# Optimization experiments

Hardware: AMD Instinct MI355X
Metric: run time of the kernel (lower is better)

Reference implementation:

```python
import jax, jax.numpy as jnp
import numpy as np

H = 8  # head_number
NEG = -1e30


def setup_inputs() -> dict:
    key = jax.random.key(0)
    ks = jax.random.split(key, 12)
    B, D, L = 32, 1024, 1024
    s = 1.0 / np.sqrt(D)
    x = jax.random.normal(ks[0], (B, D, L), dtype=jnp.float32)
    mask = jax.random.randint(ks[1], (B, L), 0, 2, dtype=jnp.int32)
    wq = jax.random.normal(ks[2], (D, D), dtype=jnp.float32) * s
    bq = jnp.zeros((D,), dtype=jnp.float32)
    wk = jax.random.normal(ks[3], (D, D), dtype=jnp.float32) * s
    bk = jnp.zeros((D,), dtype=jnp.float32)
    wv = jax.random.normal(ks[4], (D, D), dtype=jnp.float32) * s
    bv = jnp.zeros((D,), dtype=jnp.float32)
    wo = jax.random.normal(ks[5], (D, D), dtype=jnp.float32) * s
    bo = jnp.zeros((D,), dtype=jnp.float32)
    return {"x": x, "mask": mask, "wq": wq, "bq": bq, "wk": wk, "bk": bk,
            "wv": wv, "bv": bv, "wo": wo, "bo": bo}


def reference(x, mask, wq, bq, wk, bk, wv, bv, wo, bo):
    # x: [B, D, L]; mask: [B, L] with 1 = masked (pad). Dropout in eval mode (identity).
    B, D, L = x.shape
    dh = D // H
    scale = 1.0 / np.sqrt(dh)
    xt = jnp.swapaxes(x, 1, 2)  # [B, L, D]
    q = (xt @ wq.T + bq).reshape(B, L, H, dh)
    k = (xt @ wk.T + bk).reshape(B, L, H, dh)
    v = (xt @ wv.T + bv).reshape(B, L, H, dh)
    scores = jnp.einsum('bqhd,bkhd->bhqk', q, k) * scale  # [B, H, L, L]
    m = mask.astype(scores.dtype)[:, None, None, :]  # broadcast over heads, query pos
    scores = scores * (1.0 - m) + m * NEG
    attn = jax.nn.softmax(scores, axis=-1)
    out = jnp.einsum('bhqk,bkhd->bqhd', attn, v).reshape(B, L, D)
    out = out @ wo.T + bo
    return jnp.swapaxes(out, 1, 2)  # [B, D, L]
```

## Files before the change

kernel.cpp:

```cpp
#include <hip/hip_runtime.h>
#include <hip/hip_bf16.h>

typedef __bf16 bf16_t;
typedef bf16_t bf16x8 __attribute__((ext_vector_type(8)));
typedef float f32x4 __attribute__((ext_vector_type(4)));

#define MFMA16(a, b, c) __builtin_amdgcn_mfma_f32_16x16x32_bf16(a, b, c, 0, 0, 0)
#define NEGV -1e30f

__device__ __forceinline__ unsigned short f2bf(float f) {
  union { float f; unsigned int u; } v; v.f = f;
  unsigned int r = v.u + 0x7FFFu + ((v.u >> 16) & 1u);
  return (unsigned short)(r >> 16);
}

__device__ __forceinline__ void gload16(const unsigned short* g, unsigned short* l) {
  __builtin_amdgcn_global_load_lds(
      (const __attribute__((address_space(1))) void*)g,
      (__attribute__((address_space(3))) void*)l, 16, 0, 0);
}

__global__ __launch_bounds__(256) void x_transpose(
    const float* __restrict__ x, unsigned short* __restrict__ xT)
{
  const int b = blockIdx.z;
  const int l0 = blockIdx.x * 64, d0 = blockIdx.y * 64;
  __shared__ __align__(16) unsigned short T[64][68];
  const int tid = threadIdx.x;
  const int dl = tid >> 4, lc = (tid & 15) * 4;
#pragma unroll
  for (int rep = 0; rep < 4; ++rep) {
    int d = dl + rep * 16;
    float4 v = *reinterpret_cast<const float4*>(
        x + ((size_t)b * 1024 + d0 + d) * 1024 + l0 + lc);
    ushort4 u;
    u.x = f2bf(v.x); u.y = f2bf(v.y); u.z = f2bf(v.z); u.w = f2bf(v.w);
    *reinterpret_cast<ushort4*>(&T[d][lc]) = u;
  }
  __syncthreads();
  const int dbase = (tid & 15) * 4, lbase = (tid >> 4) * 4;
  ushort4 r0 = *reinterpret_cast<const ushort4*>(&T[dbase + 0][lbase]);
  ushort4 r1 = *reinterpret_cast<const ushort4*>(&T[dbase + 1][lbase]);
  ushort4 r2 = *reinterpret_cast<const ushort4*>(&T[dbase + 2][lbase]);
  ushort4 r3 = *reinterpret_cast<const ushort4*>(&T[dbase + 3][lbase]);
  ushort4 w0 = {r0.x, r1.x, r2.x, r3.x};
  ushort4 w1 = {r0.y, r1.y, r2.y, r3.y};
  ushort4 w2 = {r0.z, r1.z, r2.z, r3.z};
  ushort4 w3 = {r0.w, r1.w, r2.w, r3.w};
  unsigned short* op = xT + ((size_t)b * 1024 + l0 + lbase) * 1024 + d0 + dbase;
  *reinterpret_cast<ushort4*>(op) = w0;
  *reinterpret_cast<ushort4*>(op + 1024) = w1;
  *reinterpret_cast<ushort4*>(op + 2048) = w2;
  *reinterpret_cast<ushort4*>(op + 3072) = w3;
}

__global__ __launch_bounds__(256) void w_convert(
    const float* __restrict__ wq, const float* __restrict__ wk,
    const float* __restrict__ wv, const float* __restrict__ wo,
    unsigned short* __restrict__ Wqkv, unsigned short* __restrict__ Wo)
{
  const int z = blockIdx.y;
  const float* src = (z == 0) ? wq : (z == 1) ? wk : (z == 2) ? wv : wo;
  unsigned short* dst = (z < 3) ? Wqkv + (size_t)z * 1048576 : Wo;
  size_t off = ((size_t)blockIdx.x * 256 + threadIdx.x) * 4;
  float4 v = *reinterpret_cast<const float4*>(src + off);
  ushort4 u = {f2bf(v.x), f2bf(v.y), f2bf(v.z), f2bf(v.w)};
  *reinterpret_cast<ushort4*>(dst + off) = u;
}

__global__ __launch_bounds__(512, 2) void qkv_gemm8(
    const unsigned short* __restrict__ xT, const unsigned short* __restrict__ Wqkv,
    const float* __restrict__ bq, const float* __restrict__ bk, const float* __restrict__ bv,
    unsigned short* __restrict__ Q, unsigned short* __restrict__ K,
    unsigned short* __restrict__ Vt)
{
  __shared__ __align__(16) unsigned short lds[2][4][8192];

  const int tid = threadIdx.x;
  const int wave = tid >> 6, lane = tid & 63;
  const int lr = lane & 15, lg = lane >> 4;
  const int wr = wave >> 2, wc = wave & 3;

  const int bid = blockIdx.x;
  const int swz = (bid & 7) * 192 + (bid >> 3);
  const int mt = swz / 12, nt = swz % 12;
  const int m0 = mt * 256, n0 = nt * 256;

  const unsigned short* Ag = xT + (size_t)m0 * 1024;
  const unsigned short* Bg = Wqkv + (size_t)n0 * 1024;

  const int srow = tid >> 2;
  const int schk = (tid & 3) * 8;

#define STAGE_HT(BUF, REG, TI)                                                 \
  {                                                                            \
    const int kt_ = ((TI) < 16 ? (TI) : 15) * 64 + (((REG)&1) * 32) + schk;    \
    const unsigned short* gp_ = (((REG) < 2) ? Ag : Bg);                       \
    _Pragma("unroll")                                                          \
    for (int j_ = 0; j_ < 2; ++j_)                                             \
      gload16(gp_ + (size_t)(j_ * 128 + srow) * 1024 + kt_,                    \
              &lds[BUF][REG][j_ * 4096 + tid * 8]);                            \
  }

#define LDA(BUF, KK, MH, AR)                                                   \
  _Pragma("unroll")                                                            \
  for (int mi_ = 0; mi_ < 4; ++mi_)                                            \
    AR[mi_] = *reinterpret_cast<const bf16x8*>(                                \
        &lds[BUF][KK][(wr * 128 + (MH)*64 + mi_ * 16 + lr) * 32 + lg * 8]);

#define LDB(BUF, KK, BR)                                                       \
  _Pragma("unroll")                                                            \
  for (int n_ = 0; n_ < 4; ++n_)                                               \
    BR[n_] = *reinterpret_cast<const bf16x8*>(                                 \
        &lds[BUF][2 + (KK)][(wc * 64 + n_ * 16 + lr) * 32 + lg * 8]);

#define MM(AR, BR, MH)                                                         \
  __builtin_amdgcn_s_setprio(1);                                               \
  _Pragma("unroll")                                                            \
  for (int mi_ = 0; mi_ < 4; ++mi_)                                            \
    _Pragma("unroll")                                                          \
    for (int n_ = 0; n_ < 4; ++n_)                                             \
      acc[(MH)*4 + mi_][n_] = MFMA16(AR[mi_], BR[n_], acc[(MH)*4 + mi_][n_]);  \
  __builtin_amdgcn_s_setprio(0);

#define BAR()                                                                  \
  {                                                                            \
    asm volatile("" ::: "memory");                                             \
    __builtin_amdgcn_s_barrier();                                              \
    asm volatile("" ::: "memory");                                             \
  }
#define VMW() asm volatile("s_waitcnt vmcnt(10)" ::: "memory")

  f32x4 acc[8][4];
#pragma unroll
  for (int m = 0; m < 8; ++m)
#pragma unroll
    for (int n = 0; n < 4; ++n) acc[m][n] = (f32x4){0.f, 0.f, 0.f, 0.f};

  STAGE_HT(0, 2, 0); STAGE_HT(0, 0, 0); STAGE_HT(0, 3, 0); STAGE_HT(0, 1, 0);
  STAGE_HT(1, 2, 1); STAGE_HT(1, 0, 1); STAGE_HT(1, 3, 1);
  VMW();
  BAR();

  for (int it = 0; it < 8; ++it) {
    const int T = 2 * it;
    bf16x8 a0[4], a1[4], b0[4], b1[4];
    LDB(0, 0, b0); LDA(0, 0, 0, a0);
    STAGE_HT(1, 1, T + 1);
    BAR();
    MM(a0, b0, 0);
    BAR();
    LDA(0, 0, 1, a1);
    STAGE_HT(0, 2, T + 2);
    BAR();
    MM(a1, b0, 1);
    VMW(); BAR();
    LDB(0, 1, b1); LDA(0, 1, 0, a0);
    STAGE_HT(0, 0, T + 2);
    BAR();
    MM(a0, b1, 0);
    BAR();
    LDA(0, 1, 1, a1);
    STAGE_HT(0, 3, T + 2);
    BAR();
    MM(a1, b1, 1);
    VMW(); BAR();
    LDB(1, 0, b0); LDA(1, 0, 0, a0);
    STAGE_HT(0, 1, T + 2);
    BAR();
    MM(a0, b0, 0);
    BAR();
    LDA(1, 0, 1, a1);
    STAGE_HT(1, 2, T + 3);
    BAR();
    MM(a1, b0, 1);
    VMW(); BAR();
    LDB(1, 1, b1); LDA(1, 1, 0, a0);
    STAGE_HT(1, 0, T + 3);
    BAR();
    MM(a0, b1, 0);
    BAR();
    LDA(1, 1, 1, a1);
    STAGE_HT(1, 3, T + 3);
    BAR();
    MM(a1, b1, 1);
    VMW(); BAR();
  }

  const int zi = n0 >> 10;
  const float* bias = (zi == 0) ? bq : (zi == 1) ? bk : bv;
  const int b = m0 >> 10;
  const int lbase = (m0 & 1023) + wr * 128;

  if (zi < 2) {
    unsigned short* op = ((zi == 0) ? Q : K);
#pragma unroll
    for (int n = 0; n < 4; ++n) {
      const int col = (n0 & 1023) + wc * 64 + n * 16 + lr;
      const int h = col >> 7, d = col & 127;
      const float bs = bias[col];
      unsigned short* hp = op + ((size_t)b * 8 + h) * 131072 + d;
#pragma unroll
      for (int m = 0; m < 8; ++m)
#pragma unroll
        for (int ii = 0; ii < 4; ++ii) {
          int l = lbase + m * 16 + lg * 4 + ii;
          hp[(size_t)l * 128] = f2bf(acc[m][n][ii] + bs);
        }
    }
  } else {
#pragma unroll
    for (int n = 0; n < 4; ++n) {
      const int col = (n0 & 1023) + wc * 64 + n * 16 + lr;
      const int h = col >> 7, d = col & 127;
      const float bs = bias[col];
      unsigned short* hp = Vt + ((size_t)b * 8 + h) * 131072 + (size_t)d * 1024;
#pragma unroll
      for (int m = 0; m < 8; ++m) {
        int l = lbase + m * 16 + lg * 4;
        ushort4 u = {f2bf(acc[m][n][0] + bs), f2bf(acc[m][n][1] + bs),
                     f2bf(acc[m][n][2] + bs), f2bf(acc[m][n][3] + bs)};
        *reinterpret_cast<ushort4*>(&hp[l]) = u;
      }
    }
  }
#undef STAGE_HT
}

__global__ __launch_bounds__(512, 2) void out_gemm8(
    const unsigned short* __restrict__ Wo, const unsigned short* __restrict__ O,
    const float* __restrict__ bo, float* __restrict__ out)
{
  __shared__ __align__(16) unsigned short lds[2][4][8192];

  const int tid = threadIdx.x;
  const int wave = tid >> 6, lane = tid & 63;
  const int lr = lane & 15, lg = lane >> 4;
  const int wr = wave >> 2, wc = wave & 3;

  const int b = blockIdx.y;
  const int bid = blockIdx.x;
  const int swz = (bid & 7) * 2 + (bid >> 3);
  const int mt = swz >> 2, nt = swz & 3;
  const int d0 = mt * 256, l0 = nt * 256;

  const unsigned short* Ag = Wo + (size_t)d0 * 1024;
  const unsigned short* Og = O + (size_t)b * 8 * 131072;

  const int srow = tid >> 2;
  const int schk = (tid & 3) * 8;

#define STAGE_HT(BUF, REG, TI)                                                 \
  {                                                                            \
    const int kt_ = ((TI) < 16 ? (TI) : 15) * 64 + (((REG)&1) * 32) + schk;    \
    if ((REG) < 2) {                                                           \
      _Pragma("unroll")                                                        \
      for (int j_ = 0; j_ < 2; ++j_)                                           \
        gload16(Ag + (size_t)(j_ * 128 + srow) * 1024 + kt_,                   \
                &lds[BUF][REG][j_ * 4096 + tid * 8]);                          \
    } else {                                                                   \
      const int h_ = kt_ >> 7, dk_ = kt_ & 127;                                \
      _Pragma("unroll")                                                        \
      for (int j_ = 0; j_ < 2; ++j_)                                           \
        gload16(Og + (size_t)h_ * 131072 +                                     \
                    (size_t)(l0 + j_ * 128 + srow) * 128 + dk_,                \
                &lds[BUF][REG][j_ * 4096 + tid * 8]);                          \
    }                                                                          \
  }

  f32x4 acc[8][4];
#pragma unroll
  for (int m = 0; m < 8; ++m)
#pragma unroll
    for (int n = 0; n < 4; ++n) acc[m][n] = (f32x4){0.f, 0.f, 0.f, 0.f};

  STAGE_HT(0, 2, 0); STAGE_HT(0, 0, 0); STAGE_HT(0, 3, 0); STAGE_HT(0, 1, 0);
  STAGE_HT(1, 2, 1); STAGE_HT(1, 0, 1); STAGE_HT(1, 3, 1);
  VMW();
  BAR();

  for (int it = 0; it < 8; ++it) {
    const int T = 2 * it;
    bf16x8 a0[4], a1[4], b0[4], b1[4];
    LDB(0, 0, b0); LDA(0, 0, 0, a0);
    STAGE_HT(1, 1, T + 1);
    BAR();
    MM(a0, b0, 0);
    BAR();
    LDA(0, 0, 1, a1);
    STAGE_HT(0, 2, T + 2);
    BAR();
    MM(a1, b0, 1);
    VMW(); BAR();
    LDB(0, 1, b1); LDA(0, 1, 0, a0);
    STAGE_HT(0, 0, T + 2);
    BAR();
    MM(a0, b1, 0);
    BAR();
    LDA(0, 1, 1, a1);
    STAGE_HT(0, 3, T + 2);
    BAR();
    MM(a1, b1, 1);
    VMW(); BAR();
    LDB(1, 0, b0); LDA(1, 0, 0, a0);
    STAGE_HT(0, 1, T + 2);
    BAR();
    MM(a0, b0, 0);
    BAR();
    LDA(1, 0, 1, a1);
    STAGE_HT(1, 2, T + 3);
    BAR();
    MM(a1, b0, 1);
    VMW(); BAR();
    LDB(1, 1, b1); LDA(1, 1, 0, a0);
    STAGE_HT(1, 0, T + 3);
    BAR();
    MM(a0, b1, 0);
    BAR();
    LDA(1, 1, 1, a1);
    STAGE_HT(1, 3, T + 3);
    BAR();
    MM(a1, b1, 1);
    VMW(); BAR();
  }

#pragma unroll
  for (int m = 0; m < 8; ++m) {
#pragma unroll
    for (int ii = 0; ii < 4; ++ii) {
      int dr = d0 + wr * 128 + m * 16 + lg * 4 + ii;
      float bs = bo[dr];
      float* orow = out + ((size_t)b * 1024 + dr) * 1024 + l0 + wc * 64 + lr;
#pragma unroll
      for (int n = 0; n < 4; ++n)
        orow[n * 16] = acc[m][n][ii] + bs;
    }
  }
#undef STAGE_HT
#undef LDA
#undef LDB
#undef MM
#undef BAR
#undef VMW
}

__global__ __launch_bounds__(256, 2) void flash_attn(
    const unsigned short* __restrict__ Q, const unsigned short* __restrict__ Kb,
    const unsigned short* __restrict__ Vt, const int* __restrict__ mask,
    unsigned short* __restrict__ O)
{
  const int tid = threadIdx.x, wave = tid >> 6, lane = tid & 63;
  const int lr = lane & 15, lg = lane >> 4;
  const int qt = blockIdx.x, h = blockIdx.y, b = blockIdx.z;
  const size_t bh = (size_t)b * 8 + h;
  const unsigned short* Qp = Q + bh * 131072;
  const unsigned short* Kp = Kb + bh * 131072;
  const unsigned short* Vp = Vt + bh * 131072;
  unsigned short* Op = O + bh * 131072;
  const int q0 = qt * 128 + wave * 32;
  const float SC2 = 0.12751744f;
  const float NEG2 = -1.442695e30f;

  __shared__ __align__(16) unsigned short Kl[2][64 * 128];
  __shared__ __align__(16) unsigned short Vl[2][128 * 64];
  __shared__ __align__(16) unsigned short plds[4][16 * 76];
  __shared__ float pen[1024];

  {
    const int4 mv = *reinterpret_cast<const int4*>(mask + b * 1024 + tid * 4);
    float4 pv;
    pv.x = mv.x ? NEG2 : 0.f; pv.y = mv.y ? NEG2 : 0.f;
    pv.z = mv.z ? NEG2 : 0.f; pv.w = mv.w ? NEG2 : 0.f;
    *reinterpret_cast<float4*>(&pen[tid * 4]) = pv;
  }

  unsigned short* myP = plds[wave];

  bf16x8 aq0[4], aq1[4];
#pragma unroll
  for (int c = 0; c < 4; ++c) {
    aq0[c] = *reinterpret_cast<const bf16x8*>(
        &Qp[(size_t)(q0 + lr) * 128 + c * 32 + lg * 8]);
    aq1[c] = *reinterpret_cast<const bf16x8*>(
        &Qp[(size_t)(q0 + 16 + lr) * 128 + c * 32 + lg * 8]);
  }

#define STAGE(bufi, ktv)                                                        \
  {                                                                             \
    _Pragma("unroll")                                                           \
    for (int i = 0; i < 4; ++i) {                                               \
      int krow = i * 16 + (tid >> 4);                                           \
      int kcb = ((tid & 15) * 16) ^ ((krow & 7) << 4);                          \
      gload16(Kp + (size_t)((ktv) + krow) * 128 + (kcb >> 1),                   \
              &Kl[bufi][i * 2048 + tid * 8]);                                   \
      int aoff = i * 4096 + tid * 16;                                           \
      int r_ = aoff >> 7;                                                       \
      int Lb = aoff ^ ((r_ & 7) << 4);                                          \
      gload16(Vp + (size_t)r_ * 1024 + (ktv) + ((Lb & 127) >> 1),               \
              &Vl[bufi][i * 2048 + tid * 8]);                                   \
    }                                                                           \
  }

#define SMAXPV(S, MR, LRN, OA)                                                  \
  {                                                                             \
    float mx = fmaxf(                                                           \
        fmaxf(fmaxf(fmaxf(S[0][0], S[0][1]), fmaxf(S[0][2], S[0][3])),          \
              fmaxf(fmaxf(S[1][0], S[1][1]), fmaxf(S[1][2], S[1][3]))),         \
        fmaxf(fmaxf(fmaxf(S[2][0], S[2][1]), fmaxf(S[2][2], S[2][3])),          \
              fmaxf(fmaxf(S[3][0], S[3][1]), fmaxf(S[3][2], S[3][3]))));        \
    mx = fmaxf(mx, __shfl_xor(mx, 16));                                         \
    mx = fmaxf(mx, __shfl_xor(mx, 32));                                         \
    if (!__all(mx <= MR + 8.0f)) {                                              \
      float mnew = fmaxf(MR, mx);                                               \
      float scq = __builtin_amdgcn_exp2f(MR - mnew);                            \
      MR = mnew;                                                                \
      LRN *= scq;                                                               \
      _Pragma("unroll")                                                         \
      for (int i = 0; i < 4; ++i) {                                             \
        float sco = __shfl(scq, lg * 4 + i);                                    \
        _Pragma("unroll")                                                       \
        for (int dt = 0; dt < 8; ++dt) OA[dt][i] *= sco;                        \
      }                                                                         \
    }                                                                           \
    float p_[4][4];                                                             \
    float ls = 0.f;                                                             \
    _Pragma("unroll")                                                           \
    for (int n = 0; n < 4; ++n) {                                               \
      _Pragma("unroll")                                                         \
      for (int i = 0; i < 4; ++i)                                               \
        p_[n][i] = __builtin_amdgcn_exp2f(S[n][i] - MR);                        \
      ls += (p_[n][0] + p_[n][1]) + (p_[n][2] + p_[n][3]);                      \
    }                                                                           \
    ls += __shfl_xor(ls, 16);                                                   \
    ls += __shfl_xor(ls, 32);                                                   \
    LRN += ls;                                                                  \
    _Pragma("unroll")                                                           \
    for (int n = 0; n < 4; ++n)                                                 \
      _Pragma("unroll")                                                         \
      for (int t2 = 0; t2 < 2; ++t2) {                                          \
        unsigned int u_;                                                        \
        asm("v_cvt_pk_bf16_f32 %0, %1, %2"                                      \
            : "=v"(u_) : "v"(p_[n][2 * t2]), "v"(p_[n][2 * t2 + 1]));           \
        *reinterpret_cast<unsigned int*>(                                       \
            &myP[lr * 76 + n * 16 + lg * 4 + t2 * 2]) = u_;                     \
      }                                                                         \
    bf16x8 pa0_ = *reinterpret_cast<const bf16x8*>(&myP[lr * 76 + lg * 8]);     \
    bf16x8 pa1_ = *reinterpret_cast<const bf16x8*>(&myP[lr * 76 + 32 + lg * 8]);\
    __builtin_amdgcn_s_setprio(1);                                              \
    _Pragma("unroll")                                                           \
    for (int dt = 0; dt < 8; ++dt) {                                            \
      const int rr = dt * 16 + lr;                                              \
      const int rsw_ = (rr & 7) << 4;                                           \
      bf16x8 bv0 = *reinterpret_cast<const bf16x8*>(                            \
          &Vl[cur][(rr * 128 + ((lg * 16) ^ rsw_)) >> 1]);                      \
      bf16x8 bv1 = *reinterpret_cast<const bf16x8*>(                            \
          &Vl[cur][(rr * 128 + ((64 + lg * 16) ^ rsw_)) >> 1]);                 \
      OA[dt] = MFMA16(pa0_, bv0, OA[dt]);                                       \
      OA[dt] = MFMA16(pa1_, bv1, OA[dt]);                                       \
    }                                                                           \
    __builtin_amdgcn_s_setprio(0);                                              \
  }

  f32x4 oacc0[8], oacc1[8];
#pragma unroll
  for (int dt = 0; dt < 8; ++dt) {
    oacc0[dt] = (f32x4){0.f, 0.f, 0.f, 0.f};
    oacc1[dt] = (f32x4){0.f, 0.f, 0.f, 0.f};
  }
  float mrun0 = -3.0e38f, lrun0 = 0.f;
  float mrun1 = -3.0e38f, lrun1 = 0.f;

  STAGE(0, 0);
  __syncthreads();

  int cur = 0;
  for (int t = 0; t < 16; ++t) {
    const int kt = t * 64;
    if (t < 15) STAGE(cur ^ 1, kt + 64);

    f32x4 s0[4], s1[4];
    __builtin_amdgcn_s_setprio(1);
#pragma unroll
    for (int n = 0; n < 4; ++n) {
      const int krow = n * 16 + lr;
      const int rsw = (krow & 7) << 4;
      f32x4 a0 = (f32x4){0.f, 0.f, 0.f, 0.f};
      f32x4 a1 = (f32x4){0.f, 0.f, 0.f, 0.f};
#pragma unroll
      for (int c = 0; c < 4; ++c) {
        bf16x8 bk = *reinterpret_cast<const bf16x8*>(
            &Kl[cur][krow * 128 + (((c * 64 + lg * 16) ^ rsw) >> 1)]);
        a0 = MFMA16(bk, aq0[c], a0);
        a1 = MFMA16(bk, aq1[c], a1);
      }
      s0[n] = a0;
      s1[n] = a1;
    }
    __builtin_amdgcn_s_setprio(0);

#pragma unroll
    for (int n = 0; n < 4; ++n) {
      f32x4 pv = *reinterpret_cast<const f32x4*>(&pen[kt + n * 16 + lg * 4]);
#pragma unroll
      for (int i = 0; i < 4; ++i) {
        s0[n][i] = s0[n][i] * SC2 + pv[i];
        s1[n][i] = s1[n][i] * SC2 + pv[i];
      }
    }

    SMAXPV(s0, mrun0, lrun0, oacc0);
    SMAXPV(s1, mrun1, lrun1, oacc1);

    __syncthreads();
    cur ^= 1;
  }

  float linv0[4], linv1[4];
#pragma unroll
  for (int i = 0; i < 4; ++i) {
    linv0[i] = 1.0f / __shfl(lrun0, lg * 4 + i);
    linv1[i] = 1.0f / __shfl(lrun1, lg * 4 + i);
  }
#pragma unroll
  for (int dt = 0; dt < 8; ++dt)
#pragma unroll
    for (int i = 0; i < 4; ++i) {
      Op[(size_t)(q0 + lg * 4 + i) * 128 + dt * 16 + lr] =
          f2bf(oacc0[dt][i] * linv0[i]);
      Op[(size_t)(q0 + 16 + lg * 4 + i) * 128 + dt * 16 + lr] =
          f2bf(oacc1[dt][i] * linv1[i]);
    }
#undef STAGE
#undef SMAXPV
}

__global__ __launch_bounds__(256) void qkv_proj_old(
    const float* __restrict__ x,
    const float* __restrict__ wq, const float* __restrict__ wk, const float* __restrict__ wv,
    const float* __restrict__ bq, const float* __restrict__ bk, const float* __restrict__ bv,
    unsigned short* __restrict__ Q, unsigned short* __restrict__ K, unsigned short* __restrict__ Vt)
{
  const int tid = threadIdx.x;
  const int wave = tid >> 6, lane = tid & 63;
  const int lr = lane & 15, lg = lane >> 4;
  const int wr = wave >> 1, wc = wave & 1;
  const int mt = blockIdx.x & 7, nt = blockIdx.x >> 3;
  const int b = blockIdx.y, z = blockIdx.z;
  const int l0 = mt * 128, i0 = nt * 128;
  const float* w    = (z == 0) ? wq : (z == 1) ? wk : wv;
  const float* bias = (z == 0) ? bq : (z == 1) ? bk : bv;
  unsigned short* outp = (z == 0) ? Q : (z == 1) ? K : Vt;

  __shared__ __align__(16) unsigned short lA[128 * 40];
  __shared__ __align__(16) unsigned short lB[128 * 40];

  f32x4 acc[4][4];
#pragma unroll
  for (int m = 0; m < 4; ++m)
#pragma unroll
    for (int n = 0; n < 4; ++n) acc[m][n] = (f32x4){0.f, 0.f, 0.f, 0.f};

  const int ad = tid >> 3, aj = tid & 7;
  const int br = tid >> 1, bh2 = tid & 1;

  for (int k0 = 0; k0 < 1024; k0 += 32) {
    const float* xp = x + ((size_t)b * 1024 + k0 + ad) * 1024 + l0;
#pragma unroll
    for (int rep = 0; rep < 4; ++rep) {
      float4 v = *reinterpret_cast<const float4*>(xp + aj * 4 + rep * 32);
      int lb = aj * 4 + rep * 32;
      lA[(lb + 0) * 40 + ad] = f2bf(v.x);
      lA[(lb + 1) * 40 + ad] = f2bf(v.y);
      lA[(lb + 2) * 40 + ad] = f2bf(v.z);
      lA[(lb + 3) * 40 + ad] = f2bf(v.w);
    }
    const float* wp = w + (size_t)(i0 + br) * 1024 + k0 + bh2 * 16;
#pragma unroll
    for (int rep = 0; rep < 4; ++rep) {
      float4 v = *reinterpret_cast<const float4*>(wp + rep * 4);
      int cb = br * 40 + bh2 * 16 + rep * 4;
      lB[cb + 0] = f2bf(v.x); lB[cb + 1] = f2bf(v.y);
      lB[cb + 2] = f2bf(v.z); lB[cb + 3] = f2bf(v.w);
    }
    __syncthreads();
    bf16x8 af[4], bfr[4];
#pragma unroll
    for (int m = 0; m < 4; ++m)
      af[m] = *reinterpret_cast<const bf16x8*>(&lA[(wr * 64 + m * 16 + lr) * 40 + lg * 8]);
#pragma unroll
    for (int n = 0; n < 4; ++n)
      bfr[n] = *reinterpret_cast<const bf16x8*>(&lB[(wc * 64 + n * 16 + lr) * 40 + lg * 8]);
#pragma unroll
    for (int m = 0; m < 4; ++m)
#pragma unroll
      for (int n = 0; n < 4; ++n)
        acc[m][n] = MFMA16(af[m], bfr[n], acc[m][n]);
    __syncthreads();
  }
#pragma unroll
  for (int n = 0; n < 4; ++n) {
    int col = i0 + wc * 64 + n * 16 + lr;
    float bs = bias[col];
    int h = col >> 7, d = col & 127;
#pragma unroll
    for (int m = 0; m < 4; ++m) {
#pragma unroll
      for (int ii = 0; ii < 4; ++ii) {
        int row = l0 + wr * 64 + m * 16 + lg * 4 + ii;
        unsigned short val = f2bf(acc[m][n][ii] + bs);
        if (z < 2)
          outp[(((size_t)b * 8 + h) * 1024 + row) * 128 + d] = val;
        else
          outp[(((size_t)b * 8 + h) * 128 + d) * 1024 + row] = val;
      }
    }
  }
}

__global__ __launch_bounds__(256) void out_proj_old(
    const unsigned short* __restrict__ Obuf, const float* __restrict__ wo,
    const float* __restrict__ bo, float* __restrict__ out)
{
  const int tid = threadIdx.x, wave = tid >> 6, lane = tid & 63;
  const int lr = lane & 15, lg = lane >> 4;
  const int wr = wave >> 1, wc = wave & 1;
  const int mt = blockIdx.x & 7, nt = blockIdx.x >> 3;
  const int b = blockIdx.y;
  const int d0 = mt * 128, l0 = nt * 128;

  __shared__ __align__(16) unsigned short lA[128 * 40];
  __shared__ __align__(16) unsigned short lB[128 * 40];

  f32x4 acc[4][4];
#pragma unroll
  for (int m = 0; m < 4; ++m)
#pragma unroll
    for (int n = 0; n < 4; ++n) acc[m][n] = (f32x4){0.f, 0.f, 0.f, 0.f};

  const int ar = tid >> 1, ah = tid & 1;

  for (int k0 = 0; k0 < 1024; k0 += 32) {
    const float* wp = wo + (size_t)(d0 + ar) * 1024 + k0 + ah * 16;
#pragma unroll
    for (int rep = 0; rep < 4; ++rep) {
      float4 v = *reinterpret_cast<const float4*>(wp + rep * 4);
      int cb = ar * 40 + ah * 16 + rep * 4;
      lA[cb + 0] = f2bf(v.x); lA[cb + 1] = f2bf(v.y);
      lA[cb + 2] = f2bf(v.z); lA[cb + 3] = f2bf(v.w);
    }
    {
      int head = k0 >> 7, dk = (k0 & 127) + ah * 16;
      const unsigned short* op =
          Obuf + (((size_t)b * 8 + head) * 1024 + l0 + ar) * 128 + dk;
#pragma unroll
      for (int rep = 0; rep < 2; ++rep) {
        bf16x8 v = *reinterpret_cast<const bf16x8*>(op + rep * 8);
        *reinterpret_cast<bf16x8*>(&lB[ar * 40 + ah * 16 + rep * 8]) = v;
      }
    }
    __syncthreads();
    bf16x8 af[4], bfr[4];
#pragma unroll
    for (int m = 0; m < 4; ++m)
      af[m] = *reinterpret_cast<const bf16x8*>(&lA[(wr * 64 + m * 16 + lr) * 40 + lg * 8]);
#pragma unroll
    for (int n = 0; n < 4; ++n)
      bfr[n] = *reinterpret_cast<const bf16x8*>(&lB[(wc * 64 + n * 16 + lr) * 40 + lg * 8]);
#pragma unroll
    for (int m = 0; m < 4; ++m)
#pragma unroll
      for (int n = 0; n < 4; ++n)
        acc[m][n] = MFMA16(af[m], bfr[n], acc[m][n]);
    __syncthreads();
  }
#pragma unroll
  for (int m = 0; m < 4; ++m) {
#pragma unroll
    for (int ii = 0; ii < 4; ++ii) {
      int dr = d0 + wr * 64 + m * 16 + lg * 4 + ii;
      float bs = bo[dr];
      float* orow = out + ((size_t)b * 1024 + dr) * 1024 + l0 + wc * 64 + lr;
#pragma unroll
      for (int n = 0; n < 4; ++n)
        orow[n * 16] = acc[m][n][ii] + bs;
    }
  }
}

extern "C" void kernel_launch(void* const* d_in, const int* in_sizes, int n_in,
                              void* d_out, int out_size, void* d_ws, size_t ws_size,
                              hipStream_t stream) {
  const float* x  = (const float*)d_in[0];
  const int* mask = (const int*)d_in[1];
  const float* wq = (const float*)d_in[2];
  const float* bq = (const float*)d_in[3];
  const float* wk = (const float*)d_in[4];
  const float* bk = (const float*)d_in[5];
  const float* wv = (const float*)d_in[6];
  const float* bv = (const float*)d_in[7];
  const float* wo = (const float*)d_in[8];
  const float* bo = (const float*)d_in[9];
  float* out = (float*)d_out;

  const size_t MB64 = (size_t)64 << 20;
  const size_t NEED = (size_t)264 << 20;

  if (ws_size >= NEED) {
    unsigned short* xT   = (unsigned short*)d_ws;
    unsigned short* Q    = (unsigned short*)((char*)d_ws + MB64);
    unsigned short* K    = (unsigned short*)((char*)d_ws + 2 * MB64);
    unsigned short* Vt   = (unsigned short*)((char*)d_ws + 3 * MB64);
    unsigned short* Wqkv = (unsigned short*)((char*)d_ws + 4 * MB64);
    unsigned short* Wo   = Wqkv + (size_t)3 * 1048576;

    x_transpose<<<dim3(16, 16, 32), 256, 0, stream>>>(x, xT);
    w_convert<<<dim3(1024, 4), 256, 0, stream>>>(wq, wk, wv, wo, Wqkv, Wo);
    qkv_gemm8<<<dim3(1536), 512, 0, stream>>>(xT, Wqkv, bq, bk, bv, Q, K, Vt);
    flash_attn<<<dim3(8, 8, 32), 256, 0, stream>>>(Q, K, Vt, mask, Q);
    out_gemm8<<<dim3(16, 32), 512, 0, stream>>>(Wo, Q, bo, out);
  } else {
    unsigned short* Q  = (unsigned short*)d_ws;
    unsigned short* K  = Q + (size_t)33554432;
    unsigned short* Vt = K + (size_t)33554432;
    qkv_proj_old<<<dim3(64, 32, 3), 256, 0, stream>>>(x, wq, wk, wv, bq, bk, bv, Q, K, Vt);
    flash_attn<<<dim3(8, 8, 32), 256, 0, stream>>>(Q, K, Vt, mask, Q);
    out_proj_old<<<dim3(64, 32), 256, 0, stream>>>(Q, wo, bo, out);
  }
}
```

Measured before the change: 600.9 us.

## Single-buffer flash-attn LDS with register staging to fit three blocks per CU

```diff
diff --git a/kernel.cpp b/kernel.cpp
--- a/kernel.cpp
+++ b/kernel.cpp
@@ -344,7 +344,7 @@
 #undef VMW
 }
 
-__global__ __launch_bounds__(256, 2) void flash_attn(
+__global__ __launch_bounds__(256, 3) void flash_attn(
     const unsigned short* __restrict__ Q, const unsigned short* __restrict__ Kb,
     const unsigned short* __restrict__ Vt, const int* __restrict__ mask,
     unsigned short* __restrict__ O)
@@ -361,8 +361,8 @@
   const float SC2 = 0.12751744f;
   const float NEG2 = -1.442695e30f;
 
-  __shared__ __align__(16) unsigned short Kl[2][64 * 128];
-  __shared__ __align__(16) unsigned short Vl[2][128 * 64];
+  __shared__ __align__(16) unsigned short Kl[64 * 128];
+  __shared__ __align__(16) unsigned short Vl[128 * 64];
   __shared__ __align__(16) unsigned short plds[4][16 * 76];
   __shared__ float pen[1024];
 
@@ -385,19 +385,32 @@
         &Qp[(size_t)(q0 + 16 + lr) * 128 + c * 32 + lg * 8]);
   }
 
-#define STAGE(bufi, ktv)                                                        \
+  int4 kst[4], vst[4];
+
+#define ISSUE(ktv)                                                              \
   {                                                                             \
     _Pragma("unroll")                                                           \
     for (int i = 0; i < 4; ++i) {                                               \
-      int krow = i * 16 + (tid >> 4);                                           \
-      int kcb = ((tid & 15) * 16) ^ ((krow & 7) << 4);                          \
-      gload16(Kp + (size_t)((ktv) + krow) * 128 + (kcb >> 1),                   \
-              &Kl[bufi][i * 2048 + tid * 8]);                                   \
-      int aoff = i * 4096 + tid * 16;                                           \
-      int r_ = aoff >> 7;                                                       \
-      int Lb = aoff ^ ((r_ & 7) << 4);                                          \
-      gload16(Vp + (size_t)r_ * 1024 + (ktv) + ((Lb & 127) >> 1),               \
-              &Vl[bufi][i * 2048 + tid * 8]);                                   \
+      kst[i] = *reinterpret_cast<const int4*>(                                  \
+          Kp + (size_t)((ktv) + i * 16 + (tid >> 4)) * 128 + (tid & 15) * 8);   \
+      vst[i] = *reinterpret_cast<const int4*>(                                  \
+          Vp + (size_t)(i * 32 + (tid >> 3)) * 1024 + (ktv) + (tid & 7) * 8);   \
+    }                                                                           \
+    asm volatile("" ::: "memory");                                              \
+  }
+
+#define WRITE()                                                                 \
+  {                                                                             \
+    _Pragma("unroll")                                                           \
+    for (int i = 0; i < 4; ++i) {                                               \
+      int ok = i * 4096 + tid * 16;                                             \
+      int rk = ok >> 8;                                                         \
+      ok ^= (rk & 7) << 4;                                                      \
+      *reinterpret_cast<int4*>(&Kl[ok >> 1]) = kst[i];                          \
+      int ov = i * 4096 + tid * 16;                                             \
+      int rv = ov >> 7;                                                         \
+      ov ^= (rv & 7) << 4;                                                      \
+      *reinterpret_cast<int4*>(&Vl[ov >> 1]) = vst[i];                          \
     }                                                                           \
   }
 
@@ -452,9 +465,9 @@
       const int rr = dt * 16 + lr;                                              \
       const int rsw_ = (rr & 7) << 4;                                           \
       bf16x8 bv0 = *reinterpret_cast<const bf16x8*>(                            \
-          &Vl[cur][(rr * 128 + ((lg * 16) ^ rsw_)) >> 1]);                      \
+          &Vl[(rr * 128 + ((lg * 16) ^ rsw_)) >> 1]);                           \
       bf16x8 bv1 = *reinterpret_cast<const bf16x8*>(                            \
-          &Vl[cur][(rr * 128 + ((64 + lg * 16) ^ rsw_)) >> 1]);                 \
+          &Vl[(rr * 128 + ((64 + lg * 16) ^ rsw_)) >> 1]);                      \
       OA[dt] = MFMA16(pa0_, bv0, OA[dt]);                                       \
       OA[dt] = MFMA16(pa1_, bv1, OA[dt]);                                       \
     }                                                                           \
@@ -470,13 +483,13 @@
   float mrun0 = -3.0e38f, lrun0 = 0.f;
   float mrun1 = -3.0e38f, lrun1 = 0.f;
 
-  STAGE(0, 0);
+  ISSUE(0);
+  WRITE();
   __syncthreads();
 
-  int cur = 0;
   for (int t = 0; t < 16; ++t) {
     const int kt = t * 64;
-    if (t < 15) STAGE(cur ^ 1, kt + 64);
+    if (t < 15) ISSUE(kt + 64);
 
     f32x4 s0[4], s1[4];
     __builtin_amdgcn_s_setprio(1);
@@ -489,7 +502,7 @@
 #pragma unroll
       for (int c = 0; c < 4; ++c) {
         bf16x8 bk = *reinterpret_cast<const bf16x8*>(
-            &Kl[cur][krow * 128 + (((c * 64 + lg * 16) ^ rsw) >> 1)]);
+            &Kl[krow * 128 + (((c * 64 + lg * 16) ^ rsw) >> 1)]);
         a0 = MFMA16(bk, aq0[c], a0);
         a1 = MFMA16(bk, aq1[c], a1);
       }
@@ -512,7 +525,10 @@
     SMAXPV(s1, mrun1, lrun1, oacc1);
 
     __syncthreads();
-    cur ^= 1;
+    if (t < 15) {
+      WRITE();
+      __syncthreads();
+    }
   }
 
   float linv0[4], linv1[4];
@@ -530,7 +546,8 @@
       Op[(size_t)(q0 + 16 + lg * 4 + i) * 128 + dt * 16 + lr] =
           f2bf(oacc1[dt][i] * linv1[i]);
     }
-#undef STAGE
+#undef ISSUE
+#undef WRITE
 #undef SMAXPV
 }
 
```

Result: slower. 1.056 ms (+75.7%).
